# Kernel optimization log

Measured on AMD Instinct MI355X. Metric: run time of the kernel, lower is better.

The kernel has to match this reference:

```python
import jax, jax.numpy as jnp
import numpy as np

B, C, LQ, D = 4096, 64, 32, 128
H = 192  # 1.5 * dim
MARGIN = 1.0
EPS = 1e-12


def l2norm(x):
    return x * jax.lax.rsqrt(jnp.maximum(jnp.sum(x * x, axis=1, keepdims=True), EPS))


def setup_inputs() -> dict:
    key = jax.random.key(0)
    ks = jax.random.split(key, 16)
    question_word_embs = jax.random.normal(ks[0], (B, LQ, D), jnp.float32)
    question_lengths = jax.random.randint(ks[1], (B,), 1, LQ + 1, jnp.int32)
    header_embs = jax.random.normal(ks[2], (B, C, D), jnp.float32)
    table_word_embs = jax.random.normal(ks[3], (B, C, D), jnp.float32)
    num_cols = jax.random.randint(ks[4], (B,), 1, C + 1, jnp.int32)
    masks = (jnp.arange(C)[None, :] < num_cols[:, None]).astype(jnp.float32)
    labels = (jax.random.uniform(ks[5], (B,)) < 0.5).astype(jnp.float32)
    # table_encoder_dense: Dense(1.5*dim, relu) -> Dense(dim, relu)
    W1 = jax.random.normal(ks[6], (2 * D, H), jnp.float32) / np.sqrt(2 * D)
    b1 = jnp.zeros((H,), jnp.float32)
    W2 = jax.random.normal(ks[7], (H, D), jnp.float32) / np.sqrt(H)
    b2 = jnp.zeros((D,), jnp.float32)
    # query LSTM(dim, activation='relu'): gate order i, f, c, o (Keras)
    Wx = jax.random.normal(ks[8], (D, 4 * D), jnp.float32) / np.sqrt(D)
    Wh = jax.random.normal(ks[9], (D, 4 * D), jnp.float32) / np.sqrt(D)
    b_lstm = jnp.zeros((4 * D,), jnp.float32)
    return dict(question_word_embs=question_word_embs, question_lengths=question_lengths,
                header_embs=header_embs, table_word_embs=table_word_embs,
                num_cols=num_cols, masks=masks, labels=labels,
                W1=W1, b1=b1, W2=W2, b2=b2, Wx=Wx, Wh=Wh, b_lstm=b_lstm)


def masked_lstm(x, lengths, Wx, Wh, b):
    # x: [B, L, D]; returns final hidden state at each row's true length
    xs = jnp.transpose(x, (1, 0, 2))  # [L, B, D]
    h0 = jnp.zeros((x.shape[0], D), x.dtype)
    c0 = jnp.zeros_like(h0)

    def step(carry, inp):
        h, c = carry
        t, x_t = inp
        z = x_t @ Wx + h @ Wh + b  # [B, 4D]
        i, f, g, o = jnp.split(z, 4, axis=1)
        i = jax.nn.sigmoid(i)
        f = jax.nn.sigmoid(f)
        g = jax.nn.relu(g)           # activation='relu'
        o = jax.nn.sigmoid(o)
        c_new = f * c + i * g
        h_new = o * jax.nn.relu(c_new)
        m = (t < lengths)[:, None].astype(x_t.dtype)
        return (m * h_new + (1 - m) * h, m * c_new + (1 - m) * c), None

    (h, _), _ = jax.lax.scan(step, (h0, c0), (jnp.arange(xs.shape[0]), xs))
    return h


def reference(question_word_embs, question_lengths, header_embs, table_word_embs,
              num_cols, masks, labels, W1, b1, W2, b2, Wx, Wh, b_lstm):
    # ---- table path ----
    flat = jnp.concatenate([header_embs.reshape(-1, D), table_word_embs.reshape(-1, D)], axis=1)  # [B*C, 2D]
    h = jax.nn.relu(flat @ W1 + b1)
    te = jax.nn.relu(h @ W2 + b2).reshape(B, C, D)
    te = te * masks[:, :, None]
    te = jnp.sum(te, axis=1) / num_cols.astype(jnp.float32)[:, None]
    te = l2norm(te)
    # ---- query path (ragged-word LSTM encoder) ----
    qe = masked_lstm(question_word_embs, question_lengths, Wx, Wh, b_lstm)
    qe = l2norm(qe)
    # ---- contrastive loss ----
    d = jnp.sum(jnp.square(qe - te), axis=1)
    d_sqrt = jnp.sqrt(d)
    loss = labels * d + (1.0 - labels) * jnp.square(jnp.maximum(0.0, MARGIN - d_sqrt))
    return 0.5 * jnp.mean(loss)
```

## Files before the change

kernel.cpp:

```cpp
#include <hip/hip_runtime.h>
#include <math.h>

#define B_  4096
#define C_  64
#define LQ_ 32
#define D_  128
#define H_  192

typedef __attribute__((ext_vector_type(8))) short bf16x8;
typedef __attribute__((ext_vector_type(4))) float f32x4;

#define KEEP(x) asm volatile("" : "+v"(x))

__device__ inline unsigned cvt_pk_bf16(float lo, float hi) {
    unsigned r;
    asm("v_cvt_pk_bf16_f32 %0, %1, %2" : "=v"(r) : "v"(lo), "v"(hi));
    return r;
}
__device__ inline short f2b(float x) { return (short)(cvt_pk_bf16(x, x) & 0xffff); }
__device__ inline float sigm(float x) { return 1.f / (1.f + __expf(-x)); }

__device__ inline void wg_barrier() {
    asm volatile("s_waitcnt lgkmcnt(0)" ::: "memory");
    __builtin_amdgcn_s_barrier();
    asm volatile("" ::: "memory");
}

__global__ __launch_bounds__(256) void prep_kernel(
    const float* __restrict__ W1, const float* __restrict__ W2,
    const float* __restrict__ Wx, const float* __restrict__ Wh,
    short* __restrict__ W1T, short* __restrict__ W2T, short* __restrict__ WTl)
{
    int idx = blockIdx.x * 256 + threadIdx.x;
    if (idx < 192 * 256) {
        int j = idx >> 8, k = idx & 255;
        W1T[idx] = f2b(W1[k * H_ + j]);
    }
    if (idx < 128 * 192) {
        int j = idx / 192, k = idx - j * 192;
        W2T[idx] = f2b(W2[k * D_ + j]);
    }
    if (idx < 512 * 256) {
        int p = idx >> 8, k = idx & 255;
        int w = p >> 6, g = (p >> 4) & 3, jj = p & 15;
        int jo = g * 128 + w * 16 + jj;
        float v = (k < 128) ? Wx[k * 512 + jo] : Wh[(k - 128) * 512 + jo];
        WTl[idx] = f2b(v);
    }
}

__global__ __launch_bounds__(512) __attribute__((amdgpu_waves_per_eu(1, 2)))
void table_kernel(
    const float* __restrict__ header, const float* __restrict__ tword,
    const float* __restrict__ masks, const int* __restrict__ num_cols,
    const short* __restrict__ W1T, const float* __restrict__ b1,
    const short* __restrict__ W2T, const float* __restrict__ b2,
    float* __restrict__ te_out)
{
    const int bb0 = blockIdx.x * 16;
    const int tid = threadIdx.x;
    const int w   = tid >> 6;
    const int l   = tid & 63;
    const int lg  = l >> 4;
    const int ln  = l & 15;
    const int ww  = w & 3;
    const int wr  = w >> 2;

    __shared__ __align__(16) short flat_s[2][32 * 256];
    __shared__ __align__(16) short h_s[32 * 192];
    __shared__ float msk_s[16][64];
    __shared__ float ncol_s[16];
    __shared__ float redv2[2][128];
    __shared__ float redq[2];

    bf16x8 bw1[3][8];
    float bias1[3][4];
    #pragma unroll
    for (int ct = 0; ct < 3; ++ct) {
        int j = ww * 48 + ct * 16 + ln;
        #pragma unroll
        for (int ks = 0; ks < 8; ++ks)
            bw1[ct][ks] = *(const bf16x8*)&W1T[j * 256 + ks * 32 + lg * 8];
        #pragma unroll
        for (int reg = 0; reg < 4; ++reg)
            bias1[ct][reg] = b1[ww * 48 + ct * 16 + lg * 4 + reg];
    }
    bf16x8 bw2[2][6];
    float bias2[2][4];
    #pragma unroll
    for (int ct = 0; ct < 2; ++ct) {
        int j = ww * 32 + ct * 16 + ln;
        #pragma unroll
        for (int ks = 0; ks < 6; ++ks)
            bw2[ct][ks] = *(const bf16x8*)&W2T[j * 192 + ks * 32 + lg * 8];
        #pragma unroll
        for (int reg = 0; reg < 4; ++reg)
            bias2[ct][reg] = b2[ww * 32 + ct * 16 + lg * 4 + reg];
    }
    #pragma unroll
    for (int ct = 0; ct < 3; ++ct) {
        #pragma unroll
        for (int ks = 0; ks < 8; ++ks) KEEP(bw1[ct][ks]);
        #pragma unroll
        for (int reg = 0; reg < 4; ++reg) KEEP(bias1[ct][reg]);
    }
    #pragma unroll
    for (int ct = 0; ct < 2; ++ct) {
        #pragma unroll
        for (int ks = 0; ks < 6; ++ks) KEEP(bw2[ct][ks]);
        #pragma unroll
        for (int reg = 0; reg < 4; ++reg) KEEP(bias2[ct][reg]);
    }

    *(float2*)&((float*)msk_s)[tid * 2] =
        *(const float2*)&masks[(size_t)bb0 * C_ + tid * 2];
    if (tid < 16) ncol_s[tid] = (float)num_cols[bb0 + tid];
    __syncthreads();

    float4 pf0[4], pf1[4];
    auto issue = [&](int cc, float4 (&dst)[4]) {
        int b    = bb0 + (cc >> 1);
        int row0 = (cc & 1) * 32;
        #pragma unroll
        for (int i = 0; i < 4; ++i) {
            int idx = i * 512 + tid;
            int r   = idx >> 6;
            int c   = idx & 63;
            const float* src = (c < 32)
                ? &header[((size_t)b * C_ + row0 + r) * D_ + c * 4]
                : &tword [((size_t)b * C_ + row0 + r) * D_ + (c - 32) * 4];
            dst[i] = *(const float4*)src;
        }
    };
    issue(0, pf0);
    issue(1, pf1);

    float csum[2][4] = {{0.f, 0.f, 0.f, 0.f}, {0.f, 0.f, 0.f, 0.f}};
    const int row = wr * 16 + ln;
    const int swz = (row & 7) << 4;

    auto body = [&](int cc, int half, float4 (&pfc)[4], char* fbuf) {
        const int bi = cc >> 1;

        #pragma unroll
        for (int i = 0; i < 4; ++i) {
            int idx = i * 512 + tid;
            int r   = idx >> 6;
            int c   = idx & 63;
            uint2 p;
            p.x = cvt_pk_bf16(pfc[i].x, pfc[i].y);
            p.y = cvt_pk_bf16(pfc[i].z, pfc[i].w);
            *(uint2*)(fbuf + r * 512 + ((c * 8) ^ ((r & 7) << 4))) = p;
        }
        if (cc + 2 < 32) issue(cc + 2, pfc);
        wg_barrier();

        {
            f32x4 acc[3];
            #pragma unroll
            for (int ct = 0; ct < 3; ++ct)
                acc[ct] = (f32x4){bias1[ct][0], bias1[ct][1], bias1[ct][2], bias1[ct][3]};
            #pragma unroll
            for (int ks = 0; ks < 8; ++ks) {
                bf16x8 a = *(const bf16x8*)(fbuf + row * 512 + ((ks * 64 + lg * 16) ^ swz));
                #pragma unroll
                for (int ct = 0; ct < 3; ++ct)
                    acc[ct] = __builtin_amdgcn_mfma_f32_16x16x32_bf16(bw1[ct][ks], a, acc[ct], 0, 0, 0);
            }
            #pragma unroll
            for (int ct = 0; ct < 3; ++ct) {
                int col0 = ww * 48 + ct * 16 + lg * 4;
                uint2 hp;
                hp.x = cvt_pk_bf16(fmaxf(acc[ct][0], 0.f), fmaxf(acc[ct][1], 0.f));
                hp.y = cvt_pk_bf16(fmaxf(acc[ct][2], 0.f), fmaxf(acc[ct][3], 0.f));
                *(uint2*)((char*)h_s + row * 384 + ((col0 * 2) ^ swz)) = hp;
            }
        }
        wg_barrier();

        {
            f32x4 acc2[2];
            #pragma unroll
            for (int ct = 0; ct < 2; ++ct)
                acc2[ct] = (f32x4){bias2[ct][0], bias2[ct][1], bias2[ct][2], bias2[ct][3]};
            #pragma unroll
            for (int ks = 0; ks < 6; ++ks) {
                bf16x8 a = *(const bf16x8*)((char*)h_s + row * 384 + ((ks * 64 + lg * 16) ^ swz));
                #pragma unroll
                for (int ct = 0; ct < 2; ++ct)
                    acc2[ct] = __builtin_amdgcn_mfma_f32_16x16x32_bf16(bw2[ct][ks], a, acc2[ct], 0, 0, 0);
            }
            float m = msk_s[bi][half * 32 + row];
            #pragma unroll
            for (int ct = 0; ct < 2; ++ct)
                #pragma unroll
                for (int reg = 0; reg < 4; ++reg)
                    csum[ct][reg] = fmaf(fmaxf(acc2[ct][reg], 0.f), m, csum[ct][reg]);
        }

        if (half == 1) {
            #pragma unroll
            for (int s = 1; s < 16; s <<= 1)
                #pragma unroll
                for (int ct = 0; ct < 2; ++ct)
                    #pragma unroll
                    for (int reg = 0; reg < 4; ++reg)
                        csum[ct][reg] += __shfl_xor(csum[ct][reg], s, 64);
            if (ln == 0) {
                #pragma unroll
                for (int ct = 0; ct < 2; ++ct)
                    #pragma unroll
                    for (int reg = 0; reg < 4; ++reg)
                        redv2[wr][ww * 32 + ct * 16 + lg * 4 + reg] = csum[ct][reg];
            }
            wg_barrier();
            float v = 0.f;
            if (tid < 128) {
                v = (redv2[0][tid] + redv2[1][tid]) / ncol_s[bi];
                float s2 = v * v;
                #pragma unroll
                for (int sh = 1; sh < 64; sh <<= 1) s2 += __shfl_xor(s2, sh, 64);
                if (l == 0) redq[w] = s2;
            }
            wg_barrier();
            if (tid < 128) {
                float inv = rsqrtf(fmaxf(redq[0] + redq[1], 1e-12f));
                te_out[(size_t)(bb0 + bi) * D_ + tid] = v * inv;
            }
            #pragma unroll
            for (int ct = 0; ct < 2; ++ct)
                #pragma unroll
                for (int reg = 0; reg < 4; ++reg)
                    csum[ct][reg] = 0.f;
        }
    };

    for (int bi = 0; bi < 16; ++bi) {
        body(bi * 2,     0, pf0, (char*)flat_s[0]);
        body(bi * 2 + 1, 1, pf1, (char*)flat_s[1]);
    }
}

__global__ __launch_bounds__(512) __attribute__((amdgpu_waves_per_eu(1, 2)))
void lstm_kernel(
    const float* __restrict__ q, const int* __restrict__ lengths,
    const short* __restrict__ WTl, const float* __restrict__ bl,
    float* __restrict__ qe_out)
{
    const int tid = threadIdx.x;
    const int b0  = blockIdx.x * 16;
    const int w   = tid >> 6;
    const int l   = tid & 63;
    const int lg  = l >> 4;
    const int ln  = l & 15;
    const int d0  = w * 16 + lg * 4;

    __shared__ __align__(16) short xh[2][16 * 256];
    __shared__ float red8[8][16];

    bf16x8 wf[4][8];
    #pragma unroll
    for (int g = 0; g < 4; ++g)
        #pragma unroll
        for (int ks = 0; ks < 8; ++ks)
            wf[g][ks] = *(const bf16x8*)&WTl[(w * 64 + g * 16 + ln) * 256 + ks * 32 + lg * 8];
    float bias[4][4];
    #pragma unroll
    for (int g = 0; g < 4; ++g)
        #pragma unroll
        for (int reg = 0; reg < 4; ++reg)
            bias[g][reg] = bl[g * 128 + d0 + reg];
    #pragma unroll
    for (int g = 0; g < 4; ++g) {
        #pragma unroll
        for (int ks = 0; ks < 8; ++ks) KEEP(wf[g][ks]);
        #pragma unroll
        for (int reg = 0; reg < 4; ++reg) KEEP(bias[g][reg]);
    }

    float creg[4] = {0.f, 0.f, 0.f, 0.f};
    float hreg[4] = {0.f, 0.f, 0.f, 0.f};
    const int len = lengths[b0 + ln];
    const int sr = tid >> 5, sc = tid & 31;
    const float* qbase = &q[((size_t)(b0 + sr) * LQ_) * D_ + sc * 4];

    float4 qv0 = *(const float4*)&qbase[0 * D_];
    float4 qv1 = *(const float4*)&qbase[1 * D_];

    auto step = [&](int t, float4& qvc, char* buf) {
        uint2 px; px.x = cvt_pk_bf16(qvc.x, qvc.y); px.y = cvt_pk_bf16(qvc.z, qvc.w);
        *(uint2*)(buf + sr * 512 + ((sc * 8) ^ ((sr & 7) << 4))) = px;
        uint2 ph; ph.x = cvt_pk_bf16(hreg[0], hreg[1]); ph.y = cvt_pk_bf16(hreg[2], hreg[3]);
        *(uint2*)(buf + ln * 512 + ((256 + d0 * 2) ^ ((ln & 7) << 4))) = ph;
        if (t + 2 < LQ_) qvc = *(const float4*)&qbase[(size_t)(t + 2) * D_];
        wg_barrier();

        f32x4 acc[4];
        #pragma unroll
        for (int g = 0; g < 4; ++g)
            acc[g] = (f32x4){bias[g][0], bias[g][1], bias[g][2], bias[g][3]};
        #pragma unroll
        for (int ks = 0; ks < 8; ++ks) {
            bf16x8 xf = *(const bf16x8*)(buf + ln * 512 + ((ks * 64 + lg * 16) ^ ((ln & 7) << 4)));
            #pragma unroll
            for (int g = 0; g < 4; ++g)
                acc[g] = __builtin_amdgcn_mfma_f32_16x16x32_bf16(wf[g][ks], xf, acc[g], 0, 0, 0);
        }

        bool live = (t < len);
        #pragma unroll
        for (int reg = 0; reg < 4; ++reg) {
            float iv = sigm(acc[0][reg]);
            float fv = sigm(acc[1][reg]);
            float gv = fmaxf(acc[2][reg], 0.f);
            float ov = sigm(acc[3][reg]);
            float cn = fmaf(fv, creg[reg], iv * gv);
            float hn = ov * fmaxf(cn, 0.f);
            if (live) { creg[reg] = cn; hreg[reg] = hn; }
        }
    };

    for (int tt = 0; tt < LQ_; tt += 2) {
        step(tt,     qv0, (char*)xh[0]);
        step(tt + 1, qv1, (char*)xh[1]);
    }

    float sq = 0.f;
    #pragma unroll
    for (int reg = 0; reg < 4; ++reg) sq = fmaf(hreg[reg], hreg[reg], sq);
    sq += __shfl_xor(sq, 16, 64);
    sq += __shfl_xor(sq, 32, 64);
    if (l < 16) red8[w][ln] = sq;
    wg_barrier();
    float tot = 0.f;
    #pragma unroll
    for (int ww = 0; ww < 8; ++ww) tot += red8[ww][ln];
    float inv = rsqrtf(fmaxf(tot, 1e-12f));
    float4 o;
    o.x = hreg[0] * inv; o.y = hreg[1] * inv; o.z = hreg[2] * inv; o.w = hreg[3] * inv;
    *(float4*)&qe_out[(size_t)(b0 + ln) * D_ + d0] = o;
}

__global__ __launch_bounds__(64) void loss_kernel(
    const float* __restrict__ te, const float* __restrict__ qe,
    const float* __restrict__ labels, float* __restrict__ partial)
{
    const int tid = threadIdx.x;
    const int b   = blockIdx.x * 64 + tid;
    float dsum = 0.f;
    #pragma unroll 8
    for (int k4 = 0; k4 < 32; ++k4) {
        float4 a = *(const float4*)&qe[(size_t)b * D_ + k4 * 4];
        float4 c = *(const float4*)&te[(size_t)b * D_ + k4 * 4];
        float dx = a.x - c.x, dy = a.y - c.y, dz = a.z - c.z, dw = a.w - c.w;
        dsum += dx * dx + dy * dy + dz * dz + dw * dw;
    }
    float lab = labels[b];
    float ds  = sqrtf(dsum);
    float ml  = fmaxf(0.f, 1.f - ds);
    float loss = lab * dsum + (1.f - lab) * ml * ml;
    #pragma unroll
    for (int s = 32; s > 0; s >>= 1) loss += __shfl_xor(loss, s, 64);
    if (tid == 0) partial[blockIdx.x] = loss;
}

__global__ void final_kernel(const float* __restrict__ partial, float* __restrict__ out)
{
    const int tid = threadIdx.x;
    float v = partial[tid];
    #pragma unroll
    for (int s = 32; s > 0; s >>= 1) v += __shfl_xor(v, s, 64);
    if (tid == 0) out[0] = 0.5f * v / (float)B_;
}

extern "C" void kernel_launch(void* const* d_in, const int* in_sizes, int n_in,
                              void* d_out, int out_size, void* d_ws, size_t ws_size,
                              hipStream_t stream)
{
    const float* q      = (const float*)d_in[0];
    const int*   qlen   = (const int*)d_in[1];
    const float* header = (const float*)d_in[2];
    const float* tword  = (const float*)d_in[3];
    const int*   ncols  = (const int*)d_in[4];
    const float* masks  = (const float*)d_in[5];
    const float* labels = (const float*)d_in[6];
    const float* W1     = (const float*)d_in[7];
    const float* b1     = (const float*)d_in[8];
    const float* W2     = (const float*)d_in[9];
    const float* b2     = (const float*)d_in[10];
    const float* Wx     = (const float*)d_in[11];
    const float* Wh     = (const float*)d_in[12];
    const float* bl     = (const float*)d_in[13];
    float* out = (float*)d_out;

    float* te      = (float*)d_ws;
    float* qe      = te + (size_t)B_ * D_;
    float* partial = qe + (size_t)B_ * D_;
    short* W1T     = (short*)(partial + 64);
    short* W2T     = W1T + 192 * 256;
    short* WTl     = W2T + 128 * 192;

    prep_kernel<<<512, 256, 0, stream>>>(W1, W2, Wx, Wh, W1T, W2T, WTl);
    table_kernel<<<B_ / 16, 512, 0, stream>>>(header, tword, masks, ncols, W1T, b1, W2T, b2, te);
    lstm_kernel<<<B_ / 16, 512, 0, stream>>>(q, qlen, WTl, bl, qe);
    loss_kernel<<<B_ / 64, 64, 0, stream>>>(te, qe, labels, partial);
    final_kernel<<<1, 64, 0, stream>>>(partial, out);
}
```

Baseline: 168.5 us.

## Shrink table kernel blocks to four waves handling four batches each

The table kernel moves from 512-thread blocks covering 16 batch rows to 256-thread blocks covering 4 rows. Each wave now owns one 16-row tile, and the cross-wave reduction buffer is removed. This gives 1024 blocks instead of 256, for better CU fill and more blocks per CU, at the cost of reloading the register-resident weights in four times as many blocks. The LSTM step loop is also rolled into a plain loop with a single prefetch register, which shortens how far ahead the next input is fetched.

```diff
diff --git a/kernel.cpp b/kernel.cpp
--- a/kernel.cpp
+++ b/kernel.cpp
@@ -49,7 +49,7 @@
     }
 }
 
-__global__ __launch_bounds__(512) __attribute__((amdgpu_waves_per_eu(1, 2)))
+__global__ __launch_bounds__(256, 2)
 void table_kernel(
     const float* __restrict__ header, const float* __restrict__ tword,
     const float* __restrict__ masks, const int* __restrict__ num_cols,
@@ -57,45 +57,43 @@
     const short* __restrict__ W2T, const float* __restrict__ b2,
     float* __restrict__ te_out)
 {
-    const int bb0 = blockIdx.x * 16;
+    const int bb0 = blockIdx.x * 4;
     const int tid = threadIdx.x;
     const int w   = tid >> 6;
     const int l   = tid & 63;
     const int lg  = l >> 4;
     const int ln  = l & 15;
-    const int ww  = w & 3;
-    const int wr  = w >> 2;
-
-    __shared__ __align__(16) short flat_s[2][32 * 256];
-    __shared__ __align__(16) short h_s[32 * 192];
-    __shared__ float msk_s[16][64];
-    __shared__ float ncol_s[16];
-    __shared__ float redv2[2][128];
+
+    __shared__ __align__(16) short flat_s[2][16 * 256];
+    __shared__ __align__(16) short h_s[16 * 192];
+    __shared__ float msk_s[4][64];
+    __shared__ float ncol_s[4];
+    __shared__ float redv[128];
     __shared__ float redq[2];
 
     bf16x8 bw1[3][8];
     float bias1[3][4];
     #pragma unroll
     for (int ct = 0; ct < 3; ++ct) {
-        int j = ww * 48 + ct * 16 + ln;
+        int j = w * 48 + ct * 16 + ln;
         #pragma unroll
         for (int ks = 0; ks < 8; ++ks)
             bw1[ct][ks] = *(const bf16x8*)&W1T[j * 256 + ks * 32 + lg * 8];
         #pragma unroll
         for (int reg = 0; reg < 4; ++reg)
-            bias1[ct][reg] = b1[ww * 48 + ct * 16 + lg * 4 + reg];
+            bias1[ct][reg] = b1[w * 48 + ct * 16 + lg * 4 + reg];
     }
     bf16x8 bw2[2][6];
     float bias2[2][4];
     #pragma unroll
     for (int ct = 0; ct < 2; ++ct) {
-        int j = ww * 32 + ct * 16 + ln;
+        int j = w * 32 + ct * 16 + ln;
         #pragma unroll
         for (int ks = 0; ks < 6; ++ks)
             bw2[ct][ks] = *(const bf16x8*)&W2T[j * 192 + ks * 32 + lg * 8];
         #pragma unroll
         for (int reg = 0; reg < 4; ++reg)
-            bias2[ct][reg] = b2[ww * 32 + ct * 16 + lg * 4 + reg];
+            bias2[ct][reg] = b2[w * 32 + ct * 16 + lg * 4 + reg];
     }
     #pragma unroll
     for (int ct = 0; ct < 3; ++ct) {
@@ -112,18 +110,17 @@
         for (int reg = 0; reg < 4; ++reg) KEEP(bias2[ct][reg]);
     }
 
-    *(float2*)&((float*)msk_s)[tid * 2] =
-        *(const float2*)&masks[(size_t)bb0 * C_ + tid * 2];
-    if (tid < 16) ncol_s[tid] = (float)num_cols[bb0 + tid];
+    ((float*)msk_s)[tid] = masks[(size_t)bb0 * C_ + tid];
+    if (tid < 4) ncol_s[tid] = (float)num_cols[bb0 + tid];
     __syncthreads();
 
     float4 pf0[4], pf1[4];
     auto issue = [&](int cc, float4 (&dst)[4]) {
-        int b    = bb0 + (cc >> 1);
-        int row0 = (cc & 1) * 32;
+        int b    = bb0 + (cc >> 2);
+        int row0 = (cc & 3) * 16;
         #pragma unroll
         for (int i = 0; i < 4; ++i) {
-            int idx = i * 512 + tid;
+            int idx = i * 256 + tid;
             int r   = idx >> 6;
             int c   = idx & 63;
             const float* src = (c < 32)
@@ -136,15 +133,15 @@
     issue(1, pf1);
 
     float csum[2][4] = {{0.f, 0.f, 0.f, 0.f}, {0.f, 0.f, 0.f, 0.f}};
-    const int row = wr * 16 + ln;
-    const int swz = (row & 7) << 4;
-
-    auto body = [&](int cc, int half, float4 (&pfc)[4], char* fbuf) {
-        const int bi = cc >> 1;
+    const int row = ln;
+    const int swz = (ln & 7) << 4;
+
+    auto body = [&](int cc, float4 (&pfc)[4], char* fbuf) {
+        const int bi = cc >> 2;
 
         #pragma unroll
         for (int i = 0; i < 4; ++i) {
-            int idx = i * 512 + tid;
+            int idx = i * 256 + tid;
             int r   = idx >> 6;
             int c   = idx & 63;
             uint2 p;
@@ -152,7 +149,7 @@
             p.y = cvt_pk_bf16(pfc[i].z, pfc[i].w);
             *(uint2*)(fbuf + r * 512 + ((c * 8) ^ ((r & 7) << 4))) = p;
         }
-        if (cc + 2 < 32) issue(cc + 2, pfc);
+        if (cc + 2 < 16) issue(cc + 2, pfc);
         wg_barrier();
 
         {
@@ -169,7 +166,7 @@
             }
             #pragma unroll
             for (int ct = 0; ct < 3; ++ct) {
-                int col0 = ww * 48 + ct * 16 + lg * 4;
+                int col0 = w * 48 + ct * 16 + lg * 4;
                 uint2 hp;
                 hp.x = cvt_pk_bf16(fmaxf(acc[ct][0], 0.f), fmaxf(acc[ct][1], 0.f));
                 hp.y = cvt_pk_bf16(fmaxf(acc[ct][2], 0.f), fmaxf(acc[ct][3], 0.f));
@@ -190,7 +187,7 @@
                 for (int ct = 0; ct < 2; ++ct)
                     acc2[ct] = __builtin_amdgcn_mfma_f32_16x16x32_bf16(bw2[ct][ks], a, acc2[ct], 0, 0, 0);
             }
-            float m = msk_s[bi][half * 32 + row];
+            float m = msk_s[bi][(cc & 3) * 16 + ln];
             #pragma unroll
             for (int ct = 0; ct < 2; ++ct)
                 #pragma unroll
@@ -198,7 +195,7 @@
                     csum[ct][reg] = fmaf(fmaxf(acc2[ct][reg], 0.f), m, csum[ct][reg]);
         }
 
-        if (half == 1) {
+        if ((cc & 3) == 3) {
             #pragma unroll
             for (int s = 1; s < 16; s <<= 1)
                 #pragma unroll
@@ -211,12 +208,12 @@
                 for (int ct = 0; ct < 2; ++ct)
                     #pragma unroll
                     for (int reg = 0; reg < 4; ++reg)
-                        redv2[wr][ww * 32 + ct * 16 + lg * 4 + reg] = csum[ct][reg];
+                        redv[w * 32 + ct * 16 + lg * 4 + reg] = csum[ct][reg];
             }
             wg_barrier();
             float v = 0.f;
             if (tid < 128) {
-                v = (redv2[0][tid] + redv2[1][tid]) / ncol_s[bi];
+                v = redv[tid] / ncol_s[bi];
                 float s2 = v * v;
                 #pragma unroll
                 for (int sh = 1; sh < 64; sh <<= 1) s2 += __shfl_xor(s2, sh, 64);
@@ -235,9 +232,9 @@
         }
     };
 
-    for (int bi = 0; bi < 16; ++bi) {
-        body(bi * 2,     0, pf0, (char*)flat_s[0]);
-        body(bi * 2 + 1, 1, pf1, (char*)flat_s[1]);
+    for (int p = 0; p < 8; ++p) {
+        body(p * 2,     pf0, (char*)flat_s[0]);
+        body(p * 2 + 1, pf1, (char*)flat_s[1]);
     }
 }
 
@@ -282,17 +279,17 @@
     float hreg[4] = {0.f, 0.f, 0.f, 0.f};
     const int len = lengths[b0 + ln];
     const int sr = tid >> 5, sc = tid & 31;
-    const float* qbase = &q[((size_t)(b0 + sr) * LQ_) * D_ + sc * 4];
-
-    float4 qv0 = *(const float4*)&qbase[0 * D_];
-    float4 qv1 = *(const float4*)&qbase[1 * D_];
-
-    auto step = [&](int t, float4& qvc, char* buf) {
-        uint2 px; px.x = cvt_pk_bf16(qvc.x, qvc.y); px.y = cvt_pk_bf16(qvc.z, qvc.w);
+
+    float4 qv = *(const float4*)&q[((size_t)(b0 + sr) * LQ_ + 0) * D_ + sc * 4];
+
+    for (int t = 0; t < LQ_; ++t) {
+        char* buf = (char*)xh[t & 1];
+        uint2 px; px.x = cvt_pk_bf16(qv.x, qv.y); px.y = cvt_pk_bf16(qv.z, qv.w);
         *(uint2*)(buf + sr * 512 + ((sc * 8) ^ ((sr & 7) << 4))) = px;
         uint2 ph; ph.x = cvt_pk_bf16(hreg[0], hreg[1]); ph.y = cvt_pk_bf16(hreg[2], hreg[3]);
         *(uint2*)(buf + ln * 512 + ((256 + d0 * 2) ^ ((ln & 7) << 4))) = ph;
-        if (t + 2 < LQ_) qvc = *(const float4*)&qbase[(size_t)(t + 2) * D_];
+        if (t + 1 < LQ_)
+            qv = *(const float4*)&q[((size_t)(b0 + sr) * LQ_ + (t + 1)) * D_ + sc * 4];
         wg_barrier();
 
         f32x4 acc[4];
@@ -318,11 +315,6 @@
             float hn = ov * fmaxf(cn, 0.f);
             if (live) { creg[reg] = cn; hreg[reg] = hn; }
         }
-    };
-
-    for (int tt = 0; tt < LQ_; tt += 2) {
-        step(tt,     qv0, (char*)xh[0]);
-        step(tt + 1, qv1, (char*)xh[1]);
     }
 
     float sq = 0.f;
@@ -401,7 +393,7 @@
     short* WTl     = W2T + 128 * 192;
 
     prep_kernel<<<512, 256, 0, stream>>>(W1, W2, Wx, Wh, W1T, W2T, WTl);
-    table_kernel<<<B_ / 16, 512, 0, stream>>>(header, tword, masks, ncols, W1T, b1, W2T, b2, te);
+    table_kernel<<<B_ / 4, 256, 0, stream>>>(header, tword, masks, ncols, W1T, b1, W2T, b2, te);
     lstm_kernel<<<B_ / 16, 512, 0, stream>>>(q, qlen, WTl, bl, qe);
     loss_kernel<<<B_ / 64, 64, 0, stream>>>(te, qe, labels, partial);
     final_kernel<<<1, 64, 0, stream>>>(partial, out);
```

New measurement: 150.8 us. -10.5%, faster.
